# Kernel tuning notes

Measured on AMD Instinct MI355X. Metric: run time of the kernel, lower is better.

Reference implementation:

```python
import jax, jax.numpy as jnp
import numpy as np

N = 50000
E = 800000
D_IN, D_HID, D_OUT = 256, 256, 128


def _xavier(key, shape):
    fan_in, fan_out = shape
    limit = float(np.sqrt(6.0 / (fan_in + fan_out)))
    return jax.random.uniform(key, shape, jnp.float32, -limit, limit)


def setup_inputs() -> dict:
    key = jax.random.key(0)
    ks = jax.random.split(key, 12)
    x = jax.random.normal(ks[0], (N, D_IN), jnp.float32)
    edge_index = jax.random.randint(ks[1], (2, E), 0, N, dtype=jnp.int64)
    batch = jnp.zeros((N,), jnp.int64)
    # per-layer: message weight W, linear weight LW (stored [in, out]), bias b
    w1 = _xavier(ks[2], (D_IN, D_HID))
    lw1 = _xavier(ks[3], (D_IN, D_HID))
    lb1 = jnp.zeros((D_HID,), jnp.float32)
    w2 = _xavier(ks[4], (D_HID, D_HID))
    lw2 = _xavier(ks[5], (D_HID, D_HID))
    lb2 = jnp.zeros((D_HID,), jnp.float32)
    w3 = _xavier(ks[6], (D_HID, D_OUT))
    lw3 = _xavier(ks[7], (D_HID, D_OUT))
    lb3 = jnp.zeros((D_OUT,), jnp.float32)
    return {"x": x, "edge_index": edge_index, "batch": batch,
            "w1": w1, "lw1": lw1, "lb1": lb1,
            "w2": w2, "lw2": lw2, "lb2": lb2,
            "w3": w3, "lw3": lw3, "lb3": lb3}


def _gcn_layer(x, W, LW, b, row, col, norm):
    # message: norm * (x_j @ W); equivalent and cheaper: transform nodes once, gather
    xw = x @ W                                   # [N, out]
    msg = norm[:, None] * xw[row]                # [E, out]
    agg = jax.ops.segment_sum(msg, col, num_segments=x.shape[0])  # scatter-add at col
    return agg + x @ LW + b                      # residual linear path


def reference(x, edge_index, batch, w1, lw1, lb1, w2, lw2, lb2, w3, lw3, lb3):
    row, col = edge_index[0], edge_index[1]
    ones = jnp.ones((row.shape[0],), x.dtype)
    out_deg = jax.ops.segment_sum(ones, row, num_segments=N)
    in_deg = jax.ops.segment_sum(ones, col, num_segments=N)
    # inf at zero-degree nodes never gets gathered (those nodes have no edges)
    norm = out_deg[row] ** -0.5 * in_deg[col] ** -0.5  # [E]

    h = jax.nn.relu(_gcn_layer(x, w1, lw1, lb1, row, col, norm))
    h = jax.nn.relu(_gcn_layer(h, w2, lw2, lb2, row, col, norm))
    h = jax.nn.sigmoid(_gcn_layer(h, w3, lw3, lb3, row, col, norm))
    return h
```

## Files before the change

### kernel.cpp

```cpp
#include <hip/hip_runtime.h>
#include <hip/hip_bf16.h>
#include <math.h>

#define NNODES 50000
#define NEDGES 800000
#define HNB 64
#define HCHUNK (NEDGES / HNB)
#define HBINS 50176
#define SCAN_NB 196

typedef short s8v __attribute__((ext_vector_type(8)));
typedef float f4v __attribute__((ext_vector_type(4)));
using bf16 = __hip_bfloat16;

static __device__ __forceinline__ float bflo(unsigned int x) {
    union { unsigned int i; float f; } c; c.i = x << 16; return c.f;
}
static __device__ __forceinline__ float bfhi(unsigned int x) {
    union { unsigned int i; float f; } c; c.i = x & 0xffff0000u; return c.f;
}

static __device__ __forceinline__ void gload16(const void* g, void* l) {
    __builtin_amdgcn_global_load_lds(
        (const __attribute__((address_space(1))) unsigned int*)g,
        (__attribute__((address_space(3))) unsigned int*)l, 16, 0, 0);
}


#define M1 (256 * 512)
#define M2 (256 * 512)
#define M3 (256 * 256)

__global__ __launch_bounds__(256) void k_packall(
        const float* __restrict__ w1, const float* __restrict__ lw1,
        const float* __restrict__ w2, const float* __restrict__ lw2,
        const float* __restrict__ w3, const float* __restrict__ lw3,
        bf16* __restrict__ o1, bf16* __restrict__ o2, bf16* __restrict__ o3) {
    int i = blockIdx.x * 256 + threadIdx.x;
    const float* W; const float* LW; bf16* O; int C; int j;
    if (i < M1)            { W = w1; LW = lw1; O = o1; C = 256; j = i; }
    else if (i < M1 + M2)  { W = w2; LW = lw2; O = o2; C = 256; j = i - M1; }
    else                   { W = w3; LW = lw3; O = o3; C = 128; j = i - M1 - M2; }
    int n = j >> 8, k = j & 255;
    float v = (n < C) ? W[k * C + n] : LW[k * C + (n - C)];
    O[j] = __float2bfloat16(v);
}


__global__ __launch_bounds__(256) void k_hist(const int* __restrict__ ei,
                                              ushort* __restrict__ partials,
                                              ushort* __restrict__ lrank) {
    __shared__ unsigned int h32[HBINS / 2];
    int b = blockIdx.x, row = blockIdx.y, t = threadIdx.x;
    for (int i = t; i < HBINS / 2; i += 256) h32[i] = 0;
    __syncthreads();
    int beg = b * HCHUNK, end = beg + HCHUNK;
    const int* p = ei + (size_t)row * NEDGES;
    if (row == 0) {
        for (int e = beg + t; e < end; e += 256) {
            int id = p[e];
            atomicAdd(&h32[id >> 1], 1u << (16 * (id & 1)));
        }
    } else {
        for (int e = beg + t; e < end; e += 256) {
            int id = p[e];
            unsigned int old = atomicAdd(&h32[id >> 1], 1u << (16 * (id & 1)));
            lrank[e] = (ushort)((old >> (16 * (id & 1))) & 0xffffu);
        }
    }
    __syncthreads();
    unsigned int* o32 = (unsigned int*)(partials + ((size_t)row * HNB + b) * HBINS);
    for (int i = t; i < HBINS / 2; i += 256) o32[i] = h32[i];
}

__global__ __launch_bounds__(256) void k_hist_reduce(ushort* __restrict__ partials,
                                                     float* __restrict__ rsqrt_out,
                                                     int* __restrict__ in_cnt,
                                                     int* __restrict__ block_sums) {
    __shared__ int sm[256];
    int row = blockIdx.y;
    int i = blockIdx.x * 256 + threadIdx.x;
    if (row == 0) {
        const ushort* p = partials + i;
        int s = 0;
#pragma unroll 4
        for (int b = 0; b < HNB; ++b) s += p[(size_t)b * HBINS];
        if (i < NNODES) rsqrt_out[i] = (s > 0) ? rsqrtf((float)s) : 0.f;
    } else {
        ushort* p = partials + (size_t)HNB * HBINS + i;
        int run = 0;
        for (int b = 0; b < HNB; ++b) {
            int c = p[(size_t)b * HBINS];
            p[(size_t)b * HBINS] = (ushort)run;
            run += c;
        }
        if (i < NNODES) in_cnt[i] = run;
        sm[threadIdx.x] = (i < NNODES) ? run : 0;
        __syncthreads();
        for (int off = 128; off > 0; off >>= 1) {
            if (threadIdx.x < off) sm[threadIdx.x] += sm[threadIdx.x + off];
            __syncthreads();
        }
        if (threadIdx.x == 0) block_sums[blockIdx.x] = sm[0];
    }
}


__global__ void k_scan_blocks(const int* __restrict__ block_sums, int* __restrict__ block_base, int nb) {
    __shared__ int s[256];
    int t = threadIdx.x;
    int v = (t < nb) ? block_sums[t] : 0;
    s[t] = v;
    __syncthreads();
    for (int off = 1; off < 256; off <<= 1) {
        int u = (t >= off) ? s[t - off] : 0;
        __syncthreads();
        s[t] += u;
        __syncthreads();
    }
    block_base[t] = s[t] - v;
}

__global__ void k_scan_final(const int* __restrict__ in_cnt, const int* __restrict__ block_base,
                             int* __restrict__ offsets) {
    __shared__ int s[256];
    int b = blockIdx.x, t = threadIdx.x;
    int i = b * 256 + t;
    int v = (i < NNODES) ? in_cnt[i] : 0;
    s[t] = v;
    __syncthreads();
    for (int off = 1; off < 256; off <<= 1) {
        int u = (t >= off) ? s[t - off] : 0;
        __syncthreads();
        s[t] += u;
        __syncthreads();
    }
    int excl = s[t] - v + block_base[b];
    if (i < NNODES) offsets[i] = excl;
    if (i == NNODES - 1) offsets[NNODES] = excl + v;
}

__global__ __launch_bounds__(256) void k_scatter_free(const int* __restrict__ ei,
                                                      const int* __restrict__ offsets,
                                                      const ushort* __restrict__ partials,
                                                      const ushort* __restrict__ lrank,
                                                      int* __restrict__ src_sorted) {
    int e = blockIdx.x * 256 + threadIdx.x;
    if (e < NEDGES) {
        int r = ei[e], c = ei[NEDGES + e];
        int b = e / HCHUNK;
        int pos = offsets[c] + (int)partials[(size_t)(HNB + b) * HBINS + c] + (int)lrank[e];
        src_sorted[pos] = r;
    }
}

template<int D, int ACT>
__global__ __launch_bounds__(64) void k_agg_fused(const bf16* __restrict__ xw,
                                                  const bf16* __restrict__ xlw,
                                                  const int* __restrict__ offsets,
                                                  const int* __restrict__ src_sorted,
                                                  const float* __restrict__ bias,
                                                  void* __restrict__ out) {
    const int L = D / 8;
    const int G = 64 / L;
    const int U = 4;
    int lane = threadIdx.x;
    int v = blockIdx.x;
    int g = lane / L, sl = lane % L;

    int beg = offsets[v], end = offsets[v + 1];
    int deg = end - beg;
    int dcap = min(deg, 64);

    int id = 0;
    if (lane < dcap) id = src_sorted[beg + lane];

    float acc[U][8];
#pragma unroll
    for (int u = 0; u < U; ++u)
#pragma unroll
        for (int c = 0; c < 8; ++c) acc[u][c] = 0.f;

    const ushort* base = (const ushort*)xw + sl * 8;

    for (int e0 = 0; e0 < dcap; e0 += G * U) {
#pragma unroll
        for (int u = 0; u < U; ++u) {
            int e = e0 + u * G + g;
            int s = __shfl(id, e & 63, 64);
            float w = (e < dcap) ? 1.f : 0.f;
            uint4 q = *(const uint4*)(base + (size_t)s * D);
            acc[u][0] += w * bflo(q.x); acc[u][1] += w * bfhi(q.x);
            acc[u][2] += w * bflo(q.y); acc[u][3] += w * bfhi(q.y);
            acc[u][4] += w * bflo(q.z); acc[u][5] += w * bfhi(q.z);
            acc[u][6] += w * bflo(q.w); acc[u][7] += w * bfhi(q.w);
        }
    }
    for (int j = beg + 64 + g; j < end; j += G) {
        int s = src_sorted[j];
        uint4 q = *(const uint4*)(base + (size_t)s * D);
        acc[0][0] += bflo(q.x); acc[0][1] += bfhi(q.x);
        acc[0][2] += bflo(q.y); acc[0][3] += bfhi(q.y);
        acc[0][4] += bflo(q.z); acc[0][5] += bfhi(q.z);
        acc[0][6] += bflo(q.w); acc[0][7] += bfhi(q.w);
    }

#pragma unroll
    for (int c = 0; c < 8; ++c) acc[0][c] = (acc[0][c] + acc[1][c]) + (acc[2][c] + acc[3][c]);
#pragma unroll
    for (int d = 32; d >= L; d >>= 1) {
#pragma unroll
        for (int c = 0; c < 8; ++c) acc[0][c] += __shfl_down(acc[0][c], d, 64);
    }

    if (lane < L) {
        float sc = (deg > 0) ? rsqrtf((float)deg) : 0.f;
        const ushort* lwp = (const ushort*)xlw + (size_t)v * D + sl * 8;
        uint4 ql = *(const uint4*)lwp;
        const float* bp = bias + sl * 8;
        float4 b0 = *(const float4*)bp, b1 = *(const float4*)(bp + 4);
        float h[8];
        h[0] = acc[0][0] * sc + bflo(ql.x) + b0.x;
        h[1] = acc[0][1] * sc + bfhi(ql.x) + b0.y;
        h[2] = acc[0][2] * sc + bflo(ql.y) + b0.z;
        h[3] = acc[0][3] * sc + bfhi(ql.y) + b0.w;
        h[4] = acc[0][4] * sc + bflo(ql.z) + b1.x;
        h[5] = acc[0][5] * sc + bfhi(ql.z) + b1.y;
        h[6] = acc[0][6] * sc + bflo(ql.w) + b1.z;
        h[7] = acc[0][7] * sc + bfhi(ql.w) + b1.w;
        if (ACT == 1) {
            union { bf16 hh[8]; uint4 u; } o;
#pragma unroll
            for (int c = 0; c < 8; ++c) o.hh[c] = __float2bfloat16(fmaxf(h[c], 0.f));
            *(uint4*)((ushort*)out + (size_t)v * D + sl * 8) = o.u;
        } else {
            float r[8];
#pragma unroll
            for (int c = 0; c < 8; ++c) r[c] = 1.f / (1.f + expf(-h[c]));
            float* op = (float*)out + (size_t)v * D + sl * 8;
            *(float4*)op = (float4){r[0], r[1], r[2], r[3]};
            *(float4*)(op + 4) = (float4){r[4], r[5], r[6], r[7]};
        }
    }
}

template<int C2, bool A_BF16>
__global__ __launch_bounds__(256) void k_gemm2(const void* __restrict__ Aptr,
                                               const bf16* __restrict__ BT,
                                               const float* __restrict__ rsq,
                                               bf16* __restrict__ XW,
                                               bf16* __restrict__ XLW) {
    constexpr int R = NNODES;
    constexpr int DH = C2 / 2;
    constexpr int GX = (NNODES + 127) / 128;
    constexpr int GY = C2 / 128;
    constexpr int NWG = GX * GY;
    __shared__ bf16 As[128 * 32];
    __shared__ bf16 Bs[128 * 32];

    int o = blockIdx.x;
    constexpr int qq = NWG / 8, rr = NWG % 8;
    int xcd = o & 7, idx = o >> 3;
    int lt = (xcd < rr ? xcd * (qq + 1) : rr * (qq + 1) + (xcd - rr) * qq) + idx;
    int r0 = (lt / GY) * 128;
    int n0 = (lt % GY) * 128;

    int t = threadIdx.x;
    int wave = t >> 6, lane = t & 63;
    int wr = wave >> 1, wc = wave & 1;

    f4v acc[4][4];
#pragma unroll
    for (int mi = 0; mi < 4; ++mi)
#pragma unroll
        for (int ni = 0; ni < 4; ++ni) acc[mi][ni] = (f4v){0.f, 0.f, 0.f, 0.f};

    int sr = t >> 2;
    int sk = (t & 3) * 8;
    int fr = t >> 1, fs = (t & 1) * 16;

    for (int k0 = 0; k0 < 256; k0 += 32) {
        if (A_BF16) {
            const bf16* Ab = (const bf16*)Aptr;
            gload16(Ab + (size_t)min(r0 + sr, R - 1) * 256 + k0 + sk,
                    (char*)As + wave * 1024);
            gload16(Ab + (size_t)min(r0 + sr + 64, R - 1) * 256 + k0 + sk,
                    (char*)As + 4096 + wave * 1024);
        } else {
            const float* Af = (const float*)Aptr + (size_t)min(r0 + fr, R - 1) * 256 + k0 + fs;
            float4 f0 = ((const float4*)Af)[0];
            float4 f1 = ((const float4*)Af)[1];
            float4 f2 = ((const float4*)Af)[2];
            float4 f3 = ((const float4*)Af)[3];
            union { bf16 h[16]; uint4 u[2]; } cv;
            cv.h[0]  = __float2bfloat16(f0.x); cv.h[1]  = __float2bfloat16(f0.y);
            cv.h[2]  = __float2bfloat16(f0.z); cv.h[3]  = __float2bfloat16(f0.w);
            cv.h[4]  = __float2bfloat16(f1.x); cv.h[5]  = __float2bfloat16(f1.y);
            cv.h[6]  = __float2bfloat16(f1.z); cv.h[7]  = __float2bfloat16(f1.w);
            cv.h[8]  = __float2bfloat16(f2.x); cv.h[9]  = __float2bfloat16(f2.y);
            cv.h[10] = __float2bfloat16(f2.z); cv.h[11] = __float2bfloat16(f2.w);
            cv.h[12] = __float2bfloat16(f3.x); cv.h[13] = __float2bfloat16(f3.y);
            cv.h[14] = __float2bfloat16(f3.z); cv.h[15] = __float2bfloat16(f3.w);
            *(uint4*)&As[fr * 32 + fs]     = cv.u[0];
            *(uint4*)&As[fr * 32 + fs + 8] = cv.u[1];
        }
        gload16(BT + (size_t)(n0 + sr) * 256 + k0 + sk,
                (char*)Bs + wave * 1024);
        gload16(BT + (size_t)(n0 + sr + 64) * 256 + k0 + sk,
                (char*)Bs + 4096 + wave * 1024);
        __syncthreads();

        int lr = lane & 15, lk = (lane >> 4) * 8;
        s8v a[4], b[4];
#pragma unroll
        for (int mi = 0; mi < 4; ++mi)
            a[mi] = *(const s8v*)&As[(wr * 64 + mi * 16 + lr) * 32 + lk];
#pragma unroll
        for (int ni = 0; ni < 4; ++ni)
            b[ni] = *(const s8v*)&Bs[(wc * 64 + ni * 16 + lr) * 32 + lk];
#pragma unroll
        for (int mi = 0; mi < 4; ++mi)
#pragma unroll
            for (int ni = 0; ni < 4; ++ni)
                acc[mi][ni] = __builtin_amdgcn_mfma_f32_16x16x32_bf16(a[mi], b[ni], acc[mi][ni], 0, 0, 0);
        __syncthreads();
    }

    bool isXW = (n0 < DH);
    bf16* OutH = isXW ? XW : XLW;
    int   c0   = isXW ? n0 : n0 - DH;

    int lr = lane & 15, lq = (lane >> 4) * 4;
#pragma unroll
    for (int mi = 0; mi < 4; ++mi) {
#pragma unroll
        for (int rj = 0; rj < 4; ++rj) {
            int grow = r0 + wr * 64 + mi * 16 + lq + rj;
            if (grow < R) {
                float s = isXW ? rsq[grow] : 1.f;
#pragma unroll
                for (int ni = 0; ni < 4; ++ni) {
                    OutH[(size_t)grow * DH + c0 + wc * 64 + ni * 16 + lr] =
                        __float2bfloat16(acc[mi][ni][rj] * s);
                }
            }
        }
    }
}


extern "C" void kernel_launch(void* const* d_in, const int* in_sizes, int n_in,
                              void* d_out, int out_size, void* d_ws, size_t ws_size,
                              hipStream_t stream) {
    const float* x   = (const float*)d_in[0];
    const int*   ei  = (const int*)d_in[1];
    const float* w1  = (const float*)d_in[3];
    const float* lw1 = (const float*)d_in[4];
    const float* lb1 = (const float*)d_in[5];
    const float* w2  = (const float*)d_in[6];
    const float* lw2 = (const float*)d_in[7];
    const float* lb2 = (const float*)d_in[8];
    const float* w3  = (const float*)d_in[9];
    const float* lw3 = (const float*)d_in[10];
    const float* lb3 = (const float*)d_in[11];
    float* out = (float*)d_out;

    char* ws = (char*)d_ws;
    size_t off = 0;
    auto alloc = [&](size_t bytes) -> void* {
        void* p = ws + off;
        off += (bytes + 255) & ~(size_t)255;
        return p;
    };
    int*    in_cnt     = (int*)alloc((size_t)HBINS * 4);
    float*  rsqrt_out  = (float*)alloc((size_t)HBINS * 4);
    int*    offsets    = (int*)alloc((size_t)(NNODES + 1) * 4);
    int*    block_sums = (int*)alloc((size_t)256 * 4);
    int*    block_base = (int*)alloc((size_t)256 * 4);
    ushort* partials   = (ushort*)alloc((size_t)2 * HNB * HBINS * 2);
    ushort* lrank      = (ushort*)alloc((size_t)NEDGES * 2);
    int*    src_sorted = (int*)alloc((size_t)NEDGES * 4);
    bf16*   wcat1      = (bf16*)alloc((size_t)256 * 512 * 2);
    bf16*   wcat2      = (bf16*)alloc((size_t)256 * 512 * 2);
    bf16*   wcat3      = (bf16*)alloc((size_t)256 * 256 * 2);
    bf16*   xw         = (bf16*)alloc((size_t)NNODES * 256 * 2);
    bf16*   xlw        = (bf16*)alloc((size_t)NNODES * 256 * 2);
    bf16*   h1         = (bf16*)alloc((size_t)NNODES * 256 * 2);
    bf16*   h2         = (bf16*)alloc((size_t)NNODES * 256 * 2);

    k_packall<<<(M1 + M2 + M3) / 256, 256, 0, stream>>>(
        w1, lw1, w2, lw2, w3, lw3, wcat1, wcat2, wcat3);

    k_hist<<<dim3(HNB, 2), 256, 0, stream>>>(ei, partials, lrank);
    k_hist_reduce<<<dim3(SCAN_NB, 2), 256, 0, stream>>>(partials, rsqrt_out, in_cnt, block_sums);
    k_scan_blocks<<<1, 256, 0, stream>>>(block_sums, block_base, SCAN_NB);
    k_scan_final<<<SCAN_NB, 256, 0, stream>>>(in_cnt, block_base, offsets);
    int eblocks = (NEDGES + 255) / 256;
    k_scatter_free<<<eblocks, 256, 0, stream>>>(ei, offsets, partials, lrank, src_sorted);

    k_gemm2<512, false><<<391 * 4, 256, 0, stream>>>(x, wcat1, rsqrt_out, xw, xlw);
    k_agg_fused<256, 1><<<NNODES, 64, 0, stream>>>(xw, xlw, offsets, src_sorted, lb1, h1);
    k_gemm2<512, true><<<391 * 4, 256, 0, stream>>>(h1, wcat2, rsqrt_out, xw, xlw);
    k_agg_fused<256, 1><<<NNODES, 64, 0, stream>>>(xw, xlw, offsets, src_sorted, lb2, h2);
    k_gemm2<256, true><<<391 * 2, 256, 0, stream>>>(h2, wcat3, rsqrt_out, xw, xlw);
    k_agg_fused<128, 2><<<NNODES, 64, 0, stream>>>(xw, xlw, offsets, src_sorted, lb3, out);
}
```

Before: 406.3 us.

## Double-buffer LDS tiles in GEMM to overlap global loads with MFMA

New measurement: 419.7 us. 3.3% more time.

```diff
diff --git a/kernel.cpp b/kernel.cpp
--- a/kernel.cpp
+++ b/kernel.cpp
@@ -255,8 +255,8 @@
     constexpr int GX = (NNODES + 127) / 128;
     constexpr int GY = C2 / 128;
     constexpr int NWG = GX * GY;
-    __shared__ bf16 As[128 * 32];
-    __shared__ bf16 Bs[128 * 32];
+    __shared__ bf16 As[2][128 * 32];
+    __shared__ bf16 Bs[2][128 * 32];
 
     int o = blockIdx.x;
     constexpr int qq = NWG / 8, rr = NWG % 8;
@@ -279,19 +279,73 @@
     int sk = (t & 3) * 8;
     int fr = t >> 1, fs = (t & 1) * 16;
 
-    for (int k0 = 0; k0 < 256; k0 += 32) {
-        if (A_BF16) {
-            const bf16* Ab = (const bf16*)Aptr;
-            gload16(Ab + (size_t)min(r0 + sr, R - 1) * 256 + k0 + sk,
-                    (char*)As + wave * 1024);
-            gload16(Ab + (size_t)min(r0 + sr + 64, R - 1) * 256 + k0 + sk,
-                    (char*)As + 4096 + wave * 1024);
-        } else {
-            const float* Af = (const float*)Aptr + (size_t)min(r0 + fr, R - 1) * 256 + k0 + fs;
-            float4 f0 = ((const float4*)Af)[0];
-            float4 f1 = ((const float4*)Af)[1];
-            float4 f2 = ((const float4*)Af)[2];
-            float4 f3 = ((const float4*)Af)[3];
+    const bf16*  Ab  = (const bf16*)Aptr;
+    const float* Af0 = (const float*)Aptr;
+    float4 f0, f1, f2, f3;
+
+    if (A_BF16) {
+        gload16(Ab + (size_t)min(r0 + sr, R - 1) * 256 + sk, (char*)As[0] + wave * 1024);
+        gload16(Ab + (size_t)min(r0 + sr + 64, R - 1) * 256 + sk, (char*)As[0] + 4096 + wave * 1024);
+    } else {
+        const float* Af = Af0 + (size_t)min(r0 + fr, R - 1) * 256 + fs;
+        f0 = ((const float4*)Af)[0]; f1 = ((const float4*)Af)[1];
+        f2 = ((const float4*)Af)[2]; f3 = ((const float4*)Af)[3];
+    }
+    gload16(BT + (size_t)(n0 + sr) * 256 + sk, (char*)Bs[0] + wave * 1024);
+    gload16(BT + (size_t)(n0 + sr + 64) * 256 + sk, (char*)Bs[0] + 4096 + wave * 1024);
+    if (!A_BF16) {
+        union { bf16 h[16]; uint4 u[2]; } cv;
+        cv.h[0]  = __float2bfloat16(f0.x); cv.h[1]  = __float2bfloat16(f0.y);
+        cv.h[2]  = __float2bfloat16(f0.z); cv.h[3]  = __float2bfloat16(f0.w);
+        cv.h[4]  = __float2bfloat16(f1.x); cv.h[5]  = __float2bfloat16(f1.y);
+        cv.h[6]  = __float2bfloat16(f1.z); cv.h[7]  = __float2bfloat16(f1.w);
+        cv.h[8]  = __float2bfloat16(f2.x); cv.h[9]  = __float2bfloat16(f2.y);
+        cv.h[10] = __float2bfloat16(f2.z); cv.h[11] = __float2bfloat16(f2.w);
+        cv.h[12] = __float2bfloat16(f3.x); cv.h[13] = __float2bfloat16(f3.y);
+        cv.h[14] = __float2bfloat16(f3.z); cv.h[15] = __float2bfloat16(f3.w);
+        *(uint4*)&As[0][fr * 32 + fs]     = cv.u[0];
+        *(uint4*)&As[0][fr * 32 + fs + 8] = cv.u[1];
+    }
+    __syncthreads();
+
+    int lr = lane & 15, lk = (lane >> 4) * 8;
+
+    for (int kt = 0; kt < 8; ++kt) {
+        int cur = kt & 1, nxt = cur ^ 1;
+        int k1 = (kt + 1) * 32;
+        bool more = (kt < 7);
+
+        if (more) {
+            if (A_BF16) {
+                gload16(Ab + (size_t)min(r0 + sr, R - 1) * 256 + k1 + sk,
+                        (char*)As[nxt] + wave * 1024);
+                gload16(Ab + (size_t)min(r0 + sr + 64, R - 1) * 256 + k1 + sk,
+                        (char*)As[nxt] + 4096 + wave * 1024);
+            } else {
+                const float* Af = Af0 + (size_t)min(r0 + fr, R - 1) * 256 + k1 + fs;
+                f0 = ((const float4*)Af)[0]; f1 = ((const float4*)Af)[1];
+                f2 = ((const float4*)Af)[2]; f3 = ((const float4*)Af)[3];
+            }
+            gload16(BT + (size_t)(n0 + sr) * 256 + k1 + sk,
+                    (char*)Bs[nxt] + wave * 1024);
+            gload16(BT + (size_t)(n0 + sr + 64) * 256 + k1 + sk,
+                    (char*)Bs[nxt] + 4096 + wave * 1024);
+        }
+
+        s8v a[4], b[4];
+#pragma unroll
+        for (int mi = 0; mi < 4; ++mi)
+            a[mi] = *(const s8v*)&As[cur][(wr * 64 + mi * 16 + lr) * 32 + lk];
+#pragma unroll
+        for (int ni = 0; ni < 4; ++ni)
+            b[ni] = *(const s8v*)&Bs[cur][(wc * 64 + ni * 16 + lr) * 32 + lk];
+#pragma unroll
+        for (int mi = 0; mi < 4; ++mi)
+#pragma unroll
+            for (int ni = 0; ni < 4; ++ni)
+                acc[mi][ni] = __builtin_amdgcn_mfma_f32_16x16x32_bf16(a[mi], b[ni], acc[mi][ni], 0, 0, 0);
+
+        if (more && !A_BF16) {
             union { bf16 h[16]; uint4 u[2]; } cv;
             cv.h[0]  = __float2bfloat16(f0.x); cv.h[1]  = __float2bfloat16(f0.y);
             cv.h[2]  = __float2bfloat16(f0.z); cv.h[3]  = __float2bfloat16(f0.w);
@@ -301,28 +355,9 @@
             cv.h[10] = __float2bfloat16(f2.z); cv.h[11] = __float2bfloat16(f2.w);
             cv.h[12] = __float2bfloat16(f3.x); cv.h[13] = __float2bfloat16(f3.y);
             cv.h[14] = __float2bfloat16(f3.z); cv.h[15] = __float2bfloat16(f3.w);
-            *(uint4*)&As[fr * 32 + fs]     = cv.u[0];
-            *(uint4*)&As[fr * 32 + fs + 8] = cv.u[1];
-        }
-        gload16(BT + (size_t)(n0 + sr) * 256 + k0 + sk,
-                (char*)Bs + wave * 1024);
-        gload16(BT + (size_t)(n0 + sr + 64) * 256 + k0 + sk,
-                (char*)Bs + 4096 + wave * 1024);
-        __syncthreads();
-
-        int lr = lane & 15, lk = (lane >> 4) * 8;
-        s8v a[4], b[4];
-#pragma unroll
-        for (int mi = 0; mi < 4; ++mi)
-            a[mi] = *(const s8v*)&As[(wr * 64 + mi * 16 + lr) * 32 + lk];
-#pragma unroll
-        for (int ni = 0; ni < 4; ++ni)
-            b[ni] = *(const s8v*)&Bs[(wc * 64 + ni * 16 + lr) * 32 + lk];
-#pragma unroll
-        for (int mi = 0; mi < 4; ++mi)
-#pragma unroll
-            for (int ni = 0; ni < 4; ++ni)
-                acc[mi][ni] = __builtin_amdgcn_mfma_f32_16x16x32_bf16(a[mi], b[ni], acc[mi][ni], 0, 0, 0);
+            *(uint4*)&As[nxt][fr * 32 + fs]     = cv.u[0];
+            *(uint4*)&As[nxt][fr * 32 + fs + 8] = cv.u[1];
+        }
         __syncthreads();
     }
 
@@ -330,7 +365,7 @@
     bf16* OutH = isXW ? XW : XLW;
     int   c0   = isXW ? n0 : n0 - DH;
 
-    int lr = lane & 15, lq = (lane >> 4) * 4;
+    int lq = (lane >> 4) * 4;
 #pragma unroll
     for (int mi = 0; mi < 4; ++mi) {
 #pragma unroll
```

## Load GEMM MFMA fragments directly from global memory, dropping LDS staging

Applied to the files above, without the earlier changes.

Result: slower. 499.4 us (+22.9%).

```diff
diff --git a/kernel.cpp b/kernel.cpp
--- a/kernel.cpp
+++ b/kernel.cpp
@@ -18,12 +18,6 @@
 }
 static __device__ __forceinline__ float bfhi(unsigned int x) {
     union { unsigned int i; float f; } c; c.i = x & 0xffff0000u; return c.f;
-}
-
-static __device__ __forceinline__ void gload16(const void* g, void* l) {
-    __builtin_amdgcn_global_load_lds(
-        (const __attribute__((address_space(1))) unsigned int*)g,
-        (__attribute__((address_space(3))) unsigned int*)l, 16, 0, 0);
 }
 
 
@@ -245,7 +239,7 @@
 }
 
 template<int C2, bool A_BF16>
-__global__ __launch_bounds__(256) void k_gemm2(const void* __restrict__ Aptr,
+__global__ __launch_bounds__(256) void k_gemm3(const void* __restrict__ Aptr,
                                                const bf16* __restrict__ BT,
                                                const float* __restrict__ rsq,
                                                bf16* __restrict__ XW,
@@ -255,8 +249,6 @@
     constexpr int GX = (NNODES + 127) / 128;
     constexpr int GY = C2 / 128;
     constexpr int NWG = GX * GY;
-    __shared__ bf16 As[128 * 32];
-    __shared__ bf16 Bs[128 * 32];
 
     int o = blockIdx.x;
     constexpr int qq = NWG / 8, rr = NWG % 8;
@@ -268,6 +260,7 @@
     int t = threadIdx.x;
     int wave = t >> 6, lane = t & 63;
     int wr = wave >> 1, wc = wave & 1;
+    int lr = lane & 15, kq = (lane >> 4) * 8;
 
     f4v acc[4][4];
 #pragma unroll
@@ -275,62 +268,50 @@
 #pragma unroll
         for (int ni = 0; ni < 4; ++ni) acc[mi][ni] = (f4v){0.f, 0.f, 0.f, 0.f};
 
-    int sr = t >> 2;
-    int sk = (t & 3) * 8;
-    int fr = t >> 1, fs = (t & 1) * 16;
-
+    int arow[4], bcol[4];
+#pragma unroll
+    for (int mi = 0; mi < 4; ++mi) arow[mi] = min(r0 + wr * 64 + mi * 16 + lr, R - 1);
+#pragma unroll
+    for (int ni = 0; ni < 4; ++ni) bcol[ni] = n0 + wc * 64 + ni * 16 + lr;
+
+    const bf16*  Ab = (const bf16*)Aptr;
+    const float* Af = (const float*)Aptr;
+
+#pragma unroll 2
     for (int k0 = 0; k0 < 256; k0 += 32) {
+        s8v a[4], b[4];
+#pragma unroll
+        for (int ni = 0; ni < 4; ++ni)
+            b[ni] = *(const s8v*)(BT + (size_t)bcol[ni] * 256 + k0 + kq);
         if (A_BF16) {
-            const bf16* Ab = (const bf16*)Aptr;
-            gload16(Ab + (size_t)min(r0 + sr, R - 1) * 256 + k0 + sk,
-                    (char*)As + wave * 1024);
-            gload16(Ab + (size_t)min(r0 + sr + 64, R - 1) * 256 + k0 + sk,
-                    (char*)As + 4096 + wave * 1024);
+#pragma unroll
+            for (int mi = 0; mi < 4; ++mi)
+                a[mi] = *(const s8v*)(Ab + (size_t)arow[mi] * 256 + k0 + kq);
         } else {
-            const float* Af = (const float*)Aptr + (size_t)min(r0 + fr, R - 1) * 256 + k0 + fs;
-            float4 f0 = ((const float4*)Af)[0];
-            float4 f1 = ((const float4*)Af)[1];
-            float4 f2 = ((const float4*)Af)[2];
-            float4 f3 = ((const float4*)Af)[3];
-            union { bf16 h[16]; uint4 u[2]; } cv;
-            cv.h[0]  = __float2bfloat16(f0.x); cv.h[1]  = __float2bfloat16(f0.y);
-            cv.h[2]  = __float2bfloat16(f0.z); cv.h[3]  = __float2bfloat16(f0.w);
-            cv.h[4]  = __float2bfloat16(f1.x); cv.h[5]  = __float2bfloat16(f1.y);
-            cv.h[6]  = __float2bfloat16(f1.z); cv.h[7]  = __float2bfloat16(f1.w);
-            cv.h[8]  = __float2bfloat16(f2.x); cv.h[9]  = __float2bfloat16(f2.y);
-            cv.h[10] = __float2bfloat16(f2.z); cv.h[11] = __float2bfloat16(f2.w);
-            cv.h[12] = __float2bfloat16(f3.x); cv.h[13] = __float2bfloat16(f3.y);
-            cv.h[14] = __float2bfloat16(f3.z); cv.h[15] = __float2bfloat16(f3.w);
-            *(uint4*)&As[fr * 32 + fs]     = cv.u[0];
-            *(uint4*)&As[fr * 32 + fs + 8] = cv.u[1];
-        }
-        gload16(BT + (size_t)(n0 + sr) * 256 + k0 + sk,
-                (char*)Bs + wave * 1024);
-        gload16(BT + (size_t)(n0 + sr + 64) * 256 + k0 + sk,
-                (char*)Bs + 4096 + wave * 1024);
-        __syncthreads();
-
-        int lr = lane & 15, lk = (lane >> 4) * 8;
-        s8v a[4], b[4];
-#pragma unroll
-        for (int mi = 0; mi < 4; ++mi)
-            a[mi] = *(const s8v*)&As[(wr * 64 + mi * 16 + lr) * 32 + lk];
-#pragma unroll
-        for (int ni = 0; ni < 4; ++ni)
-            b[ni] = *(const s8v*)&Bs[(wc * 64 + ni * 16 + lr) * 32 + lk];
+#pragma unroll
+            for (int mi = 0; mi < 4; ++mi) {
+                const float4* p = (const float4*)(Af + (size_t)arow[mi] * 256 + k0 + kq);
+                float4 u0 = p[0], u1 = p[1];
+                union { bf16 h[8]; s8v v; } cv;
+                cv.h[0] = __float2bfloat16(u0.x); cv.h[1] = __float2bfloat16(u0.y);
+                cv.h[2] = __float2bfloat16(u0.z); cv.h[3] = __float2bfloat16(u0.w);
+                cv.h[4] = __float2bfloat16(u1.x); cv.h[5] = __float2bfloat16(u1.y);
+                cv.h[6] = __float2bfloat16(u1.z); cv.h[7] = __float2bfloat16(u1.w);
+                a[mi] = cv.v;
+            }
+        }
 #pragma unroll
         for (int mi = 0; mi < 4; ++mi)
 #pragma unroll
             for (int ni = 0; ni < 4; ++ni)
                 acc[mi][ni] = __builtin_amdgcn_mfma_f32_16x16x32_bf16(a[mi], b[ni], acc[mi][ni], 0, 0, 0);
-        __syncthreads();
     }
 
     bool isXW = (n0 < DH);
     bf16* OutH = isXW ? XW : XLW;
     int   c0   = isXW ? n0 : n0 - DH;
 
-    int lr = lane & 15, lq = (lane >> 4) * 4;
+    int lq = (lane >> 4) * 4;
 #pragma unroll
     for (int mi = 0; mi < 4; ++mi) {
 #pragma unroll
@@ -398,10 +379,10 @@
     int eblocks = (NEDGES + 255) / 256;
     k_scatter_free<<<eblocks, 256, 0, stream>>>(ei, offsets, partials, lrank, src_sorted);
 
-    k_gemm2<512, false><<<391 * 4, 256, 0, stream>>>(x, wcat1, rsqrt_out, xw, xlw);
+    k_gemm3<512, false><<<391 * 4, 256, 0, stream>>>(x, wcat1, rsqrt_out, xw, xlw);
     k_agg_fused<256, 1><<<NNODES, 64, 0, stream>>>(xw, xlw, offsets, src_sorted, lb1, h1);
-    k_gemm2<512, true><<<391 * 4, 256, 0, stream>>>(h1, wcat2, rsqrt_out, xw, xlw);
+    k_gemm3<512, true><<<391 * 4, 256, 0, stream>>>(h1, wcat2, rsqrt_out, xw, xlw);
     k_agg_fused<256, 1><<<NNODES, 64, 0, stream>>>(xw, xlw, offsets, src_sorted, lb2, h2);
-    k_gemm2<256, true><<<391 * 2, 256, 0, stream>>>(h2, wcat3, rsqrt_out, xw, xlw);
+    k_gemm3<256, true><<<391 * 2, 256, 0, stream>>>(h2, wcat3, rsqrt_out, xw, xlw);
     k_agg_fused<128, 2><<<NNODES, 64, 0, stream>>>(xw, xlw, offsets, src_sorted, lb3, out);
 }
```
